# Optimization experiments

Measured on AMD Instinct MI355X. Metric: run time of the kernel, lower is better.

The kernel has to match this reference:

```python
import jax, jax.numpy as jnp
import numpy as np

HEADS = 16
EMBED_DIM = 1024
HEAD_DIM = EMBED_DIM // HEADS
N, Q_LEN, KV_LEN = 4, 2048, 2048


def setup_inputs() -> dict:
    key = jax.random.key(0)
    k1, k2, k3, k4, k5, k6 = jax.random.split(key, 6)
    query = jax.random.normal(k1, (N, Q_LEN, EMBED_DIM), dtype=jnp.float32)
    key_t = jax.random.normal(k2, (N, KV_LEN, EMBED_DIM), dtype=jnp.float32)
    value = jax.random.normal(k3, (N, KV_LEN, EMBED_DIM), dtype=jnp.float32)
    mask = jax.random.randint(k4, (N, 1, Q_LEN, KV_LEN), 0, 2, dtype=jnp.int32)
    # output projection (the only Linear actually used in the original forward)
    W_out = jax.random.normal(k5, (EMBED_DIM, EMBED_DIM), dtype=jnp.float32) / np.sqrt(EMBED_DIM)
    b_out = jax.random.normal(k6, (EMBED_DIM,), dtype=jnp.float32) * 0.01
    return {"query": query, "key": key_t, "value": value, "mask": mask,
            "W_out": W_out, "b_out": b_out}


def reference(query, key, value, mask, W_out, b_out):
    n, q_len, _ = query.shape
    k_len = key.shape[1]
    # split heads: [N, L, E] -> [N, L, H, D]
    q = query.reshape(n, q_len, HEADS, HEAD_DIM)
    k = key.reshape(n, k_len, HEADS, HEAD_DIM)
    v = value.reshape(n, k_len, HEADS, HEAD_DIM)
    # full QK^T scores: [N, H, Q, K]
    scores = jnp.einsum("nqhd,nkhd->nhqk", q, k)
    scores = jnp.where(mask == 0, jnp.float32(-1e9), scores)
    # non-canonical scale: 1/sqrt(embed_dim), applied AFTER masking (as original)
    attn = jax.nn.softmax(scores / jnp.sqrt(jnp.float32(EMBED_DIM)), axis=3)
    out = jnp.einsum("nhql,nlhd->nqhd", attn, v).reshape(n, q_len, HEADS * HEAD_DIM)
    return out @ W_out.T + b_out
```

## Files before the change

### kernel.cpp

```cpp
#include <hip/hip_runtime.h>
#include <stdint.h>

#define NB 4
#define QL 2048
#define KL 2048
#define HEADS 16
#define EMB 1024
#define HD 64

typedef float f32x2 __attribute__((ext_vector_type(2)));
typedef float f32x4 __attribute__((ext_vector_type(4)));
typedef float f32x16 __attribute__((ext_vector_type(16)));
typedef __bf16 bf16x2 __attribute__((ext_vector_type(2)));
typedef __bf16 bf16x8 __attribute__((ext_vector_type(8)));
typedef unsigned short u16x8 __attribute__((ext_vector_type(8)));
typedef unsigned short u16x4 __attribute__((ext_vector_type(4)));
typedef unsigned int u32x4 __attribute__((ext_vector_type(4)));

static __device__ __forceinline__ unsigned short f2bf(float f) {
  unsigned u = __float_as_uint(f);
  u += 0x7fffu + ((u >> 16) & 1u);
  return (unsigned short)(u >> 16);
}
static __device__ __forceinline__ float bf2f(unsigned short h) {
  return __uint_as_float(((unsigned)h) << 16);
}
static __device__ __forceinline__ float fast_exp2(float x) {
#if __has_builtin(__builtin_amdgcn_exp2f)
  return __builtin_amdgcn_exp2f(x);
#else
  return __expf(x * 0.6931471805599453f);
#endif
}
static __device__ __forceinline__ float fast_rcp(float x) {
#if __has_builtin(__builtin_amdgcn_rcpf)
  return __builtin_amdgcn_rcpf(x);
#else
  return 1.0f / x;
#endif
}
static __device__ __forceinline__ void dma16(const void* g, void* l) {
  __builtin_amdgcn_global_load_lds(
      (const __attribute__((address_space(1))) unsigned int*)(uintptr_t)g,
      (__attribute__((address_space(3))) unsigned int*)(uintptr_t)l, 16, 0, 0);
}
static __device__ __forceinline__ void dma4(const void* g, void* l) {
  __builtin_amdgcn_global_load_lds(
      (const __attribute__((address_space(1))) unsigned int*)(uintptr_t)g,
      (__attribute__((address_space(3))) unsigned int*)(uintptr_t)l, 4, 0, 0);
}
static __device__ __forceinline__ void barrier_plain() {
  __asm__ volatile("" ::: "memory");
  __builtin_amdgcn_s_barrier();
  __asm__ volatile("" ::: "memory");
}
#define WAITVM(N) __asm__ volatile("s_waitcnt vmcnt(" #N ")" ::: "memory")

#define XHI_OFF  0ull
#define XLO_OFF  16777216ull
#define KHI_OFF  33554432ull
#define VT_OFF   50331648ull
#define WHI_OFF  67108864ull
#define WLO_OFF  69206016ull
#define MB_OFF   71303168ull

#define QSC  0.0450842399f
#define ESHIFT 11.5415601730f

__global__ __launch_bounds__(256) void prep_all(const float* __restrict__ Kg,
                                                const float* __restrict__ Vg,
                                                const float* __restrict__ Wg,
                                                const int* __restrict__ Mg,
                                                unsigned short* __restrict__ Khi,
                                                unsigned short* __restrict__ Vt,
                                                unsigned short* __restrict__ Whi,
                                                unsigned short* __restrict__ Wlo,
                                                unsigned long long* __restrict__ bits) {
  __shared__ unsigned short lds[64 * 66];
  const int tid = threadIdx.x;
  const int bid = blockIdx.x;
  if (bid < 8192) {
    int t = bid * 256 + tid;
    int d4 = t & 15, h = (t >> 4) & 15, kv = (t >> 8) & 2047, n = t >> 19;
    f32x4 a = *(const f32x4*)(Kg + (size_t)(n * KL + kv) * EMB + h * 64 + d4 * 4);
    u16x4 o;
    #pragma unroll
    for (int j = 0; j < 4; ++j) o[j] = f2bf(a[j]);
    int row = kv & 63, c0 = d4 >> 1;
    int pos = row * 128 + ((c0 ^ (row & 7)) << 4) + (d4 & 1) * 8;
    size_t slab = (size_t)((n * 16 + h) * 32 + (kv >> 6)) * 8192;
    *(u16x4*)((char*)Khi + slab + pos) = o;
  } else if (bid < 10240) {
    int vb = bid - 8192;
    int kt = vb & 31, h = (vb >> 5) & 15, n = vb >> 9;
    #pragma unroll
    for (int i = 0; i < 4; ++i) {
      int e = i * 256 + tid;
      int d4 = e & 15, kvl = e >> 4;
      int col = (kvl & 48) | (kvl & 3) | ((kvl & 4) << 1) | ((kvl & 8) >> 1);
      f32x4 a = *(const f32x4*)(Vg + (size_t)(n * KL + kt * 64 + kvl) * EMB + h * 64 + d4 * 4);
      #pragma unroll
      for (int j = 0; j < 4; ++j) lds[(d4 * 4 + j) * 66 + col] = f2bf(a[j]);
    }
    __syncthreads();
    size_t slab = (size_t)((n * 16 + h) * 32 + kt) * 8192;
    #pragma unroll
    for (int i = 0; i < 4; ++i) {
      int e = i * 256 + tid;
      int kv4 = e & 15, d = e >> 4;
      u16x4 o;
      #pragma unroll
      for (int j = 0; j < 4; ++j) o[j] = lds[d * 66 + kv4 * 4 + j];
      int c0 = kv4 >> 1;
      int pos = d * 128 + ((c0 ^ (d & 7)) << 4) + (kv4 & 1) * 8;
      *(u16x4*)((char*)Vt + slab + pos) = o;
    }
  } else if (bid < 11264) {
    int t = (bid - 10240) * 256 + tid;
    int c4 = t & 255, row = t >> 8;
    f32x4 a = *(const f32x4*)(Wg + (size_t)row * 1024 + c4 * 4);
    u16x4 hi, lo;
    #pragma unroll
    for (int j = 0; j < 4; ++j) {
      unsigned short hb = f2bf(a[j]);
      hi[j] = hb;
      lo[j] = f2bf(a[j] - bf2f(hb));
    }
    *(u16x4*)(Whi + (size_t)row * 1024 + c4 * 4) = hi;
    *(u16x4*)(Wlo + (size_t)row * 1024 + c4 * 4) = lo;
  } else {
    int t = (bid - 11264) * 256 + tid;
    int wd = t >> 6, lane = t & 63;
    int row = wd >> 5, kw = wd & 31;
    int v = Mg[row * KL + kw * 64 + lane];
    unsigned long long b = __ballot(v != 0);
    int q = row & 2047, nn = row >> 11;
    if (lane == 0)
      bits[((size_t)((nn * 16 + (q >> 7)) * 32 + kw)) * 128 + (q & 127)] = b;
  }
}

__global__ __launch_bounds__(256, 4) void attn3(const float* __restrict__ Qg,
                                                const unsigned short* __restrict__ Khi,
                                                const unsigned short* __restrict__ Vt,
                                                const unsigned long long* __restrict__ Mb,
                                                unsigned short* __restrict__ Xhi,
                                                unsigned short* __restrict__ Xlo) {
  __shared__ __align__(16) char smem[2 * 17408];
  const int tid = threadIdx.x;
  const int w = tid >> 6;
  const int l = tid & 63;
  const int q32 = l & 31;
  const int h5 = l >> 5;
  const int bid = blockIdx.x;
  const int qb = bid & 15;
  const int h = (bid >> 4) & 15;
  const int n = bid >> 8;
  const int q0 = qb * 128 + w * 32;

  const char* kslab = (const char*)Khi + (size_t)(n * HEADS + h) * 262144;
  const char* vslab = (const char*)Vt + (size_t)(n * HEADS + h) * 262144;
  const char* mslab = (const char*)Mb + (size_t)(n * 16 + qb) * 32768;

  bf16x8 qh[4];
  {
    const float* qp = Qg + (size_t)(n * QL + q0 + q32) * EMB + h * HD + h5 * 8;
    #pragma unroll
    for (int kc = 0; kc < 4; ++kc) {
      union { u16x8 u; bf16x8 b; } H;
      #pragma unroll
      for (int j = 0; j < 8; ++j) H.u[j] = f2bf(qp[kc * 16 + j] * QSC);
      qh[kc] = H.b;
    }
  }
  WAITVM(0);

  int off8[2][4];
  #pragma unroll
  for (int r2 = 0; r2 < 2; ++r2)
    #pragma unroll
    for (int g = 0; g < 4; ++g)
      off8[r2][g] = (r2 * 32 + q32) * 128 + (((2 * g + h5) ^ (q32 & 7)) << 4);

  f32x16 o0, o1, ol;
  #pragma unroll
  for (int i = 0; i < 16; ++i) { o0[i] = 0.f; o1[i] = 0.f; ol[i] = 0.f; }

  union { u16x8 u; bf16x8 b; } O1;
  #pragma unroll
  for (int j = 0; j < 8; ++j) O1.u[j] = 0x3F80;
  const bf16x8 ones = O1.b;

  auto issue = [&](int kt, char* buf) {
    const char* ks = kslab + kt * 8192 + w * 2048 + l * 16;
    const char* vs = vslab + kt * 8192 + w * 2048 + l * 16;
    dma16(ks, buf + w * 2048);
    dma16(ks + 1024, buf + w * 2048 + 1024);
    dma16(vs, buf + 8192 + w * 2048);
    dma16(vs + 1024, buf + 8192 + w * 2048 + 1024);
    dma4(mslab + kt * 1024 + w * 256 + l * 4, buf + 16384 + w * 256);
  };

  auto step = [&](int kt, char* cur, char* nxt) {
    barrier_plain();
    if (kt != 31) {
      issue(kt + 1, nxt);
      WAITVM(5);
    } else {
      WAITVM(0);
    }
    barrier_plain();
    uint2 mw = *(const uint2*)(cur + 16384 + w * 256 + q32 * 8);

    #pragma unroll
    for (int Mt = 0; Mt < 2; ++Mt) {
      f32x16 st;
      #pragma unroll
      for (int i = 0; i < 16; ++i) st[i] = -ESHIFT;
      #pragma unroll
      for (int kc = 0; kc < 4; ++kc) {
        union { u16x8 u; bf16x8 b; } kf;
        kf.u = *(const u16x8*)(cur + off8[Mt][kc]);
        st = __builtin_amdgcn_mfma_f32_32x32x16_bf16(kf.b, qh[kc], st, 0, 0, 0);
      }
      unsigned int half = (Mt ? mw.y : mw.x) >> (h5 * 4);
      unsigned int pk[8];
      #pragma unroll
      for (int i = 0; i < 8; ++i) {
        const int r0 = 2 * i;
        const int b0 = (r0 & 3) + 8 * (r0 >> 2);
        float a0 = ((half >> b0) & 1u) ? st[r0] : -1.0e38f;
        float a1 = ((half >> (b0 + 1)) & 1u) ? st[r0 + 1] : -1.0e38f;
        float p0 = fast_exp2(a0);
        float p1 = fast_exp2(a1);
        bf16x2 pv = __builtin_convertvector((f32x2){p0, p1}, bf16x2);
        unsigned int u;
        __builtin_memcpy(&u, &pv, 4);
        pk[i] = u;
      }
      #pragma unroll
      for (int kc2 = 0; kc2 < 2; ++kc2) {
        union { u32x4 wv; bf16x8 b; } pf;
        pf.wv[0] = pk[4 * kc2 + 0];
        pf.wv[1] = pk[4 * kc2 + 1];
        pf.wv[2] = pk[4 * kc2 + 2];
        pf.wv[3] = pk[4 * kc2 + 3];
        const int kvc = Mt * 2 + kc2;
        union { u16x8 u; bf16x8 b; } vf0, vf1;
        vf0.u = *(const u16x8*)(cur + 8192 + off8[0][kvc]);
        vf1.u = *(const u16x8*)(cur + 8192 + off8[1][kvc]);
        o0 = __builtin_amdgcn_mfma_f32_32x32x16_bf16(pf.b, vf0.b, o0, 0, 0, 0);
        o1 = __builtin_amdgcn_mfma_f32_32x32x16_bf16(pf.b, vf1.b, o1, 0, 0, 0);
        ol = __builtin_amdgcn_mfma_f32_32x32x16_bf16(pf.b, ones, ol, 0, 0, 0);
      }
    }
  };

  issue(0, smem);
  for (int kt2 = 0; kt2 < 16; ++kt2) {
    step(2 * kt2, smem, smem + 17408);
    step(2 * kt2 + 1, smem + 17408, smem);
  }

  #pragma unroll
  for (int r = 0; r < 16; ++r) {
    float inv = fast_rcp(ol[r]);
    int qr = (r & 3) + 8 * (r >> 2) + 4 * h5;
    size_t base = (size_t)(n * QL + q0 + qr) * EMB + h * HD + q32;
    float v0 = o0[r] * inv;
    unsigned short h0 = f2bf(v0);
    Xhi[base] = h0;
    Xlo[base] = f2bf(v0 - bf2f(h0));
    float v1 = o1[r] * inv;
    unsigned short h1 = f2bf(v1);
    Xhi[base + 32] = h1;
    Xlo[base + 32] = f2bf(v1 - bf2f(h1));
  }
}

__global__ __launch_bounds__(256, 2) void proj3(const unsigned short* __restrict__ Xhi,
                                                const unsigned short* __restrict__ Xlo,
                                                const unsigned short* __restrict__ Whi,
                                                const unsigned short* __restrict__ Wlo,
                                                const float* __restrict__ bias,
                                                float* __restrict__ out) {
  __shared__ __align__(16) char pm[65536];
  const int tid = threadIdx.x;
  const int w = tid >> 6;
  const int l = tid & 63;
  const int lr = l & 15;
  const int lq = l >> 4;
  const int wm = w >> 1, wn = w & 1;
  const int bid = blockIdx.x;
  const int m0 = (bid >> 3) * 128;
  const int n0 = (bid & 7) * 128;

  f32x4 acc[4][4];
  #pragma unroll
  for (int i = 0; i < 4; ++i)
    #pragma unroll
    for (int j = 0; j < 4; ++j) acc[i][j] = (f32x4){0.f, 0.f, 0.f, 0.f};

  auto issue = [&](int kc, char* buf) {
    #pragma unroll
    for (int i = 0; i < 8; ++i) {
      int s = (i * 256 + tid) * 16;
      int sel = s >> 13;
      int s2 = s & 8191;
      int row = s2 >> 6;
      int c = (s2 >> 4) & 3;
      const unsigned short* pl = sel == 0 ? Xhi : sel == 1 ? Xlo : sel == 2 ? Whi : Wlo;
      int rbase = (sel < 2 ? m0 : n0) + row;
      dma16(pl + (size_t)rbase * 1024 + kc * 32 + c * 8, buf + i * 4096 + w * 1024);
    }
  };

  auto pstep = [&](int kc, char* cur, char* nxt) {
    barrier_plain();
    if (kc != 31) {
      issue(kc + 1, nxt);
      WAITVM(8);
    } else {
      WAITVM(0);
    }
    barrier_plain();

    bf16x8 ah[4], al[4], bh[4], bl[4];
    #pragma unroll
    for (int mt = 0; mt < 4; ++mt) {
      int off = (wm * 64 + mt * 16 + lr) * 64 + lq * 16;
      union { u16x8 u; bf16x8 b; } A, B;
      A.u = *(const u16x8*)(cur + off);
      B.u = *(const u16x8*)(cur + 8192 + off);
      ah[mt] = A.b;
      al[mt] = B.b;
    }
    #pragma unroll
    for (int nt = 0; nt < 4; ++nt) {
      int off = (wn * 64 + nt * 16 + lr) * 64 + lq * 16;
      union { u16x8 u; bf16x8 b; } A, B;
      A.u = *(const u16x8*)(cur + 16384 + off);
      B.u = *(const u16x8*)(cur + 24576 + off);
      bh[nt] = A.b;
      bl[nt] = B.b;
    }
    #pragma unroll
    for (int mt = 0; mt < 4; ++mt)
      #pragma unroll
      for (int nt = 0; nt < 4; ++nt) {
        f32x4 c = acc[mt][nt];
        c = __builtin_amdgcn_mfma_f32_16x16x32_bf16(ah[mt], bh[nt], c, 0, 0, 0);
        c = __builtin_amdgcn_mfma_f32_16x16x32_bf16(ah[mt], bl[nt], c, 0, 0, 0);
        c = __builtin_amdgcn_mfma_f32_16x16x32_bf16(al[mt], bh[nt], c, 0, 0, 0);
        acc[mt][nt] = c;
      }
  };

  issue(0, pm);
  for (int kc2 = 0; kc2 < 16; ++kc2) {
    pstep(2 * kc2, pm, pm + 32768);
    pstep(2 * kc2 + 1, pm + 32768, pm);
  }

  #pragma unroll
  for (int nt = 0; nt < 4; ++nt) {
    int col = n0 + wn * 64 + nt * 16 + lr;
    float bv = bias[col];
    #pragma unroll
    for (int mt = 0; mt < 4; ++mt) {
      int rowb = m0 + wm * 64 + mt * 16 + lq * 4;
      #pragma unroll
      for (int r = 0; r < 4; ++r)
        out[(size_t)(rowb + r) * EMB + col] = acc[mt][nt][r] + bv;
    }
  }
}

extern "C" void kernel_launch(void* const* d_in, const int* in_sizes, int n_in,
                              void* d_out, int out_size, void* d_ws, size_t ws_size,
                              hipStream_t stream) {
  const float* Qg = (const float*)d_in[0];
  const float* Kg = (const float*)d_in[1];
  const float* Vg = (const float*)d_in[2];
  const int* Mg = (const int*)d_in[3];
  const float* Wg = (const float*)d_in[4];
  const float* Bg = (const float*)d_in[5];
  float* out = (float*)d_out;

  char* ws = (char*)d_ws;
  unsigned short* xhi = (unsigned short*)(ws + XHI_OFF);
  unsigned short* xlo = (unsigned short*)(ws + XLO_OFF);
  unsigned short* khi = (unsigned short*)(ws + KHI_OFF);
  unsigned short* vt = (unsigned short*)(ws + VT_OFF);
  unsigned short* whi = (unsigned short*)(ws + WHI_OFF);
  unsigned short* wlo = (unsigned short*)(ws + WLO_OFF);
  unsigned long long* mbits = (unsigned long long*)(ws + MB_OFF);

  prep_all<<<76800, 256, 0, stream>>>(Kg, Vg, Wg, Mg, khi, vt, whi, wlo, mbits);
  attn3<<<NB * HEADS * (QL / 128), 256, 0, stream>>>(Qg, khi, vt, mbits, xhi, xlo);
  proj3<<<(NB * QL / 128) * (EMB / 128), 256, 0, stream>>>(xhi, xlo, whi, wlo, Bg, out);
}
```

Measured before the change: 345.2 us.

## Process two 32-row query chunks per wave to reuse K/V tiles

```diff
diff --git a/kernel.cpp b/kernel.cpp
--- a/kernel.cpp
+++ b/kernel.cpp
@@ -130,47 +130,56 @@
     *(u16x4*)(Wlo + (size_t)row * 1024 + c4 * 4) = lo;
   } else {
     int t = (bid - 11264) * 256 + tid;
-    int wd = t >> 6, lane = t & 63;
-    int row = wd >> 5, kw = wd & 31;
-    int v = Mg[row * KL + kw * 64 + lane];
-    unsigned long long b = __ballot(v != 0);
+    int l = t & 63;
+    int W = t >> 6;
+    int kw2 = (W & 15) * 2;
+    int row = W >> 4;
+    const int* mp = Mg + (size_t)row * KL;
+    int v0 = mp[kw2 * 64 + l];
+    int v1 = mp[kw2 * 64 + 64 + l];
+    unsigned long long b0 = __ballot(v0 != 0);
+    unsigned long long b1 = __ballot(v1 != 0);
     int q = row & 2047, nn = row >> 11;
-    if (lane == 0)
-      bits[((size_t)((nn * 16 + (q >> 7)) * 32 + kw)) * 128 + (q & 127)] = b;
-  }
-}
-
-__global__ __launch_bounds__(256, 4) void attn3(const float* __restrict__ Qg,
+    size_t base = (size_t)((nn * 8 + (q >> 8)) * 32) * 256 + (q & 255);
+    if (l == 0) {
+      bits[base + (size_t)kw2 * 256] = b0;
+      bits[base + (size_t)(kw2 + 1) * 256] = b1;
+    }
+  }
+}
+
+__global__ __launch_bounds__(256, 2) void attn4(const float* __restrict__ Qg,
                                                 const unsigned short* __restrict__ Khi,
                                                 const unsigned short* __restrict__ Vt,
                                                 const unsigned long long* __restrict__ Mb,
                                                 unsigned short* __restrict__ Xhi,
                                                 unsigned short* __restrict__ Xlo) {
-  __shared__ __align__(16) char smem[2 * 17408];
+  __shared__ __align__(16) char smem[2 * 18432];
   const int tid = threadIdx.x;
   const int w = tid >> 6;
   const int l = tid & 63;
   const int q32 = l & 31;
   const int h5 = l >> 5;
   const int bid = blockIdx.x;
-  const int qb = bid & 15;
-  const int h = (bid >> 4) & 15;
-  const int n = bid >> 8;
-  const int q0 = qb * 128 + w * 32;
+  const int qb = bid & 7;
+  const int h = (bid >> 3) & 15;
+  const int n = bid >> 7;
+  const int qbase = qb * 256 + w * 64;
 
   const char* kslab = (const char*)Khi + (size_t)(n * HEADS + h) * 262144;
   const char* vslab = (const char*)Vt + (size_t)(n * HEADS + h) * 262144;
-  const char* mslab = (const char*)Mb + (size_t)(n * 16 + qb) * 32768;
-
-  bf16x8 qh[4];
-  {
-    const float* qp = Qg + (size_t)(n * QL + q0 + q32) * EMB + h * HD + h5 * 8;
+  const char* mslab = (const char*)Mb + (size_t)(n * 8 + qb) * 65536;
+
+  bf16x8 qh[2][4];
+  #pragma unroll
+  for (int c = 0; c < 2; ++c) {
+    const float* qp = Qg + (size_t)(n * QL + qbase + c * 32 + q32) * EMB + h * HD + h5 * 8;
     #pragma unroll
     for (int kc = 0; kc < 4; ++kc) {
       union { u16x8 u; bf16x8 b; } H;
       #pragma unroll
       for (int j = 0; j < 8; ++j) H.u[j] = f2bf(qp[kc * 16 + j] * QSC);
-      qh[kc] = H.b;
+      qh[c][kc] = H.b;
     }
   }
   WAITVM(0);
@@ -182,9 +191,11 @@
     for (int g = 0; g < 4; ++g)
       off8[r2][g] = (r2 * 32 + q32) * 128 + (((2 * g + h5) ^ (q32 & 7)) << 4);
 
-  f32x16 o0, o1, ol;
-  #pragma unroll
-  for (int i = 0; i < 16; ++i) { o0[i] = 0.f; o1[i] = 0.f; ol[i] = 0.f; }
+  f32x16 o00, o01, o10, o11, l0, l1;
+  #pragma unroll
+  for (int i = 0; i < 16; ++i) {
+    o00[i] = 0.f; o01[i] = 0.f; o10[i] = 0.f; o11[i] = 0.f; l0[i] = 0.f; l1[i] = 0.f;
+  }
 
   union { u16x8 u; bf16x8 b; } O1;
   #pragma unroll
@@ -198,83 +209,102 @@
     dma16(ks + 1024, buf + w * 2048 + 1024);
     dma16(vs, buf + 8192 + w * 2048);
     dma16(vs + 1024, buf + 8192 + w * 2048 + 1024);
-    dma4(mslab + kt * 1024 + w * 256 + l * 4, buf + 16384 + w * 256);
+    const char* ms = mslab + kt * 2048 + w * 512 + l * 4;
+    dma4(ms, buf + 16384 + w * 512);
+    dma4(ms + 256, buf + 16384 + w * 512 + 256);
   };
 
   auto step = [&](int kt, char* cur, char* nxt) {
     barrier_plain();
     if (kt != 31) {
       issue(kt + 1, nxt);
-      WAITVM(5);
+      WAITVM(6);
     } else {
       WAITVM(0);
     }
     barrier_plain();
-    uint2 mw = *(const uint2*)(cur + 16384 + w * 256 + q32 * 8);
+    unsigned long long mwc0 = *(const unsigned long long*)(cur + 16384 + (w * 64 + q32) * 8);
+    unsigned long long mwc1 = *(const unsigned long long*)(cur + 16384 + (w * 64 + 32 + q32) * 8);
 
     #pragma unroll
     for (int Mt = 0; Mt < 2; ++Mt) {
-      f32x16 st;
-      #pragma unroll
-      for (int i = 0; i < 16; ++i) st[i] = -ESHIFT;
-      #pragma unroll
-      for (int kc = 0; kc < 4; ++kc) {
-        union { u16x8 u; bf16x8 b; } kf;
-        kf.u = *(const u16x8*)(cur + off8[Mt][kc]);
-        st = __builtin_amdgcn_mfma_f32_32x32x16_bf16(kf.b, qh[kc], st, 0, 0, 0);
+      union { u16x8 u; bf16x8 b; } kf[4];
+      #pragma unroll
+      for (int kc = 0; kc < 4; ++kc) kf[kc].u = *(const u16x8*)(cur + off8[Mt][kc]);
+
+      unsigned int pk0[8], pk1[8];
+      #pragma unroll
+      for (int c = 0; c < 2; ++c) {
+        f32x16 st;
+        #pragma unroll
+        for (int i = 0; i < 16; ++i) st[i] = -ESHIFT;
+        #pragma unroll
+        for (int kc = 0; kc < 4; ++kc)
+          st = __builtin_amdgcn_mfma_f32_32x32x16_bf16(kf[kc].b, qh[c][kc], st, 0, 0, 0);
+        unsigned long long mwc = c ? mwc1 : mwc0;
+        unsigned int half = (unsigned int)(Mt ? (mwc >> 32) : mwc) >> (h5 * 4);
+        unsigned int* pk = c ? pk1 : pk0;
+        #pragma unroll
+        for (int i = 0; i < 8; ++i) {
+          const int r0 = 2 * i;
+          const int b0 = (r0 & 3) + 8 * (r0 >> 2);
+          float a0 = ((half >> b0) & 1u) ? st[r0] : -1.0e38f;
+          float a1 = ((half >> (b0 + 1)) & 1u) ? st[r0 + 1] : -1.0e38f;
+          float p0 = fast_exp2(a0);
+          float p1 = fast_exp2(a1);
+          bf16x2 pv = __builtin_convertvector((f32x2){p0, p1}, bf16x2);
+          unsigned int u;
+          __builtin_memcpy(&u, &pv, 4);
+          pk[i] = u;
+        }
       }
-      unsigned int half = (Mt ? mw.y : mw.x) >> (h5 * 4);
-      unsigned int pk[8];
-      #pragma unroll
-      for (int i = 0; i < 8; ++i) {
-        const int r0 = 2 * i;
-        const int b0 = (r0 & 3) + 8 * (r0 >> 2);
-        float a0 = ((half >> b0) & 1u) ? st[r0] : -1.0e38f;
-        float a1 = ((half >> (b0 + 1)) & 1u) ? st[r0 + 1] : -1.0e38f;
-        float p0 = fast_exp2(a0);
-        float p1 = fast_exp2(a1);
-        bf16x2 pv = __builtin_convertvector((f32x2){p0, p1}, bf16x2);
-        unsigned int u;
-        __builtin_memcpy(&u, &pv, 4);
-        pk[i] = u;
-      }
       #pragma unroll
       for (int kc2 = 0; kc2 < 2; ++kc2) {
-        union { u32x4 wv; bf16x8 b; } pf;
-        pf.wv[0] = pk[4 * kc2 + 0];
-        pf.wv[1] = pk[4 * kc2 + 1];
-        pf.wv[2] = pk[4 * kc2 + 2];
-        pf.wv[3] = pk[4 * kc2 + 3];
         const int kvc = Mt * 2 + kc2;
         union { u16x8 u; bf16x8 b; } vf0, vf1;
         vf0.u = *(const u16x8*)(cur + 8192 + off8[0][kvc]);
         vf1.u = *(const u16x8*)(cur + 8192 + off8[1][kvc]);
-        o0 = __builtin_amdgcn_mfma_f32_32x32x16_bf16(pf.b, vf0.b, o0, 0, 0, 0);
-        o1 = __builtin_amdgcn_mfma_f32_32x32x16_bf16(pf.b, vf1.b, o1, 0, 0, 0);
-        ol = __builtin_amdgcn_mfma_f32_32x32x16_bf16(pf.b, ones, ol, 0, 0, 0);
+        union { u32x4 wv; bf16x8 b; } pf0, pf1;
+        #pragma unroll
+        for (int j = 0; j < 4; ++j) {
+          pf0.wv[j] = pk0[4 * kc2 + j];
+          pf1.wv[j] = pk1[4 * kc2 + j];
+        }
+        o00 = __builtin_amdgcn_mfma_f32_32x32x16_bf16(pf0.b, vf0.b, o00, 0, 0, 0);
+        o01 = __builtin_amdgcn_mfma_f32_32x32x16_bf16(pf0.b, vf1.b, o01, 0, 0, 0);
+        l0  = __builtin_amdgcn_mfma_f32_32x32x16_bf16(pf0.b, ones,  l0,  0, 0, 0);
+        o10 = __builtin_amdgcn_mfma_f32_32x32x16_bf16(pf1.b, vf0.b, o10, 0, 0, 0);
+        o11 = __builtin_amdgcn_mfma_f32_32x32x16_bf16(pf1.b, vf1.b, o11, 0, 0, 0);
+        l1  = __builtin_amdgcn_mfma_f32_32x32x16_bf16(pf1.b, ones,  l1,  0, 0, 0);
       }
     }
   };
 
   issue(0, smem);
   for (int kt2 = 0; kt2 < 16; ++kt2) {
-    step(2 * kt2, smem, smem + 17408);
-    step(2 * kt2 + 1, smem + 17408, smem);
-  }
-
-  #pragma unroll
-  for (int r = 0; r < 16; ++r) {
-    float inv = fast_rcp(ol[r]);
-    int qr = (r & 3) + 8 * (r >> 2) + 4 * h5;
-    size_t base = (size_t)(n * QL + q0 + qr) * EMB + h * HD + q32;
-    float v0 = o0[r] * inv;
-    unsigned short h0 = f2bf(v0);
-    Xhi[base] = h0;
-    Xlo[base] = f2bf(v0 - bf2f(h0));
-    float v1 = o1[r] * inv;
-    unsigned short h1 = f2bf(v1);
-    Xhi[base + 32] = h1;
-    Xlo[base + 32] = f2bf(v1 - bf2f(h1));
+    step(2 * kt2, smem, smem + 18432);
+    step(2 * kt2 + 1, smem + 18432, smem);
+  }
+
+  #pragma unroll
+  for (int c = 0; c < 2; ++c) {
+    const f32x16& oa = c ? o10 : o00;
+    const f32x16& ob = c ? o11 : o01;
+    const f32x16& ll = c ? l1 : l0;
+    #pragma unroll
+    for (int r = 0; r < 16; ++r) {
+      float inv = fast_rcp(ll[r]);
+      int qr = (r & 3) + 8 * (r >> 2) + 4 * h5;
+      size_t base = (size_t)(n * QL + qbase + c * 32 + qr) * EMB + h * HD + q32;
+      float v0 = oa[r] * inv;
+      unsigned short h0 = f2bf(v0);
+      Xhi[base] = h0;
+      Xlo[base] = f2bf(v0 - bf2f(h0));
+      float v1 = ob[r] * inv;
+      unsigned short h1 = f2bf(v1);
+      Xhi[base + 32] = h1;
+      Xlo[base + 32] = f2bf(v1 - bf2f(h1));
+    }
   }
 }
 
@@ -396,7 +426,7 @@
   unsigned short* wlo = (unsigned short*)(ws + WLO_OFF);
   unsigned long long* mbits = (unsigned long long*)(ws + MB_OFF);
 
-  prep_all<<<76800, 256, 0, stream>>>(Kg, Vg, Wg, Mg, khi, vt, whi, wlo, mbits);
-  attn3<<<NB * HEADS * (QL / 128), 256, 0, stream>>>(Qg, khi, vt, mbits, xhi, xlo);
+  prep_all<<<44032, 256, 0, stream>>>(Kg, Vg, Wg, Mg, khi, vt, whi, wlo, mbits);
+  attn4<<<NB * HEADS * (QL / 256), 256, 0, stream>>>(Qg, khi, vt, mbits, xhi, xlo);
   proj3<<<(NB * QL / 128) * (EMB / 128), 256, 0, stream>>>(xhi, xlo, whi, wlo, Bg, out);
 }
```

After: 330.9 us. -4.2%, faster.
